# Optimization experiments

Measured on AMD Instinct MI355X. Metric: run time of the kernel, lower is better.

The kernel has to match this reference:

```python
import jax, jax.numpy as jnp
import numpy as np
from math import factorial

# ---- irreps metadata: 12x0e + 4x1o + 4x1e + 6x2e (dim 66) ----
GROUPS = [(12, 0), (4, 1), (4, 1), (6, 2)]  # (mul, l); parity: [e, o, e, e]

def _slices(groups):
    s, out = 0, []
    for m, l in groups:
        d = m * (2 * l + 1)
        out.append((s, s + d))
        s += d
    return out

SL = _slices(GROUPS)
DIM = SL[-1][1]                      # 66
SH_L = [0, 1, 2]
SH_SL = [(0, 1), (1, 4), (4, 9)]     # sh dim 9

# all parity/l-allowed paths (in_group, sh_idx, out_group) of the FC tensor product
PATHS = [(0, 0, 0), (0, 1, 1), (0, 2, 3),
         (1, 0, 1), (1, 1, 0), (1, 1, 2), (1, 1, 3), (1, 2, 1),
         (2, 0, 2), (2, 1, 1), (2, 2, 2), (2, 2, 3),
         (3, 0, 3), (3, 1, 1), (3, 2, 0), (3, 2, 2), (3, 2, 3)]
WEIGHT_NUMEL = sum(GROUPS[a][0] * GROUPS[c][0] for a, _, c in PATHS)  # 632
FAN = [0] * len(GROUPS)
for a, b, c in PATHS:
    FAN[c] += GROUPS[a][0]

# ---- real Clebsch-Gordan tensors ----

def _su2_cg(j1, j2, j3, m1, m2, m3):
    if m1 + m2 != m3:
        return 0.0
    f = factorial
    pre = ((2 * j3 + 1) * f(j3 + j1 - j2) * f(j3 - j1 + j2) * f(j1 + j2 - j3) / f(j1 + j2 + j3 + 1)) ** 0.5
    pre *= (f(j3 + m3) * f(j3 - m3) * f(j1 - m1) * f(j1 + m1) * f(j2 - m2) * f(j2 + m2)) ** 0.5
    s = 0.0
    for k in range(j1 + j2 - j3 + 1):
        args = (k, j1 + j2 - j3 - k, j1 - m1 - k, j2 + m2 - k, j3 - j2 + m1 + k, j3 - j1 - m2 + k)
        if min(args) < 0:
            continue
        d = 1.0
        for a in args:
            d *= f(a)
        s += (-1) ** k / d
    return pre * s

def _u_real(l):
    # complex -> real spherical-harmonic change of basis, rows m=-l..l
    U = np.zeros((2 * l + 1, 2 * l + 1), dtype=np.complex128)
    sq = 1.0 / np.sqrt(2.0)
    for m in range(-l, l + 1):
        i = m + l
        if m > 0:
            U[i, l + m] = ((-1) ** m) * sq
            U[i, l - m] = sq
        elif m == 0:
            U[i, l] = 1.0
        else:
            U[i, l + m] = 1j * sq
            U[i, l - m] = -1j * ((-1) ** m) * sq
    return U

def _real_cg(l1, l2, l3):
    Cc = np.zeros((2 * l1 + 1, 2 * l2 + 1, 2 * l3 + 1), dtype=np.complex128)
    for m1 in range(-l1, l1 + 1):
        for m2 in range(-l2, l2 + 1):
            m3 = m1 + m2
            if abs(m3) <= l3:
                Cc[l1 + m1, l2 + m2, l3 + m3] = _su2_cg(l1, l2, l3, m1, m2, m3)
    U1, U2, U3 = _u_real(l1), _u_real(l2), _u_real(l3)
    T = np.einsum('ai,bj,ck,ijk->abc', U1.conj(), U2.conj(), U3, Cc)
    T = T.real if np.abs(T.real).sum() >= np.abs(T.imag).sum() else T.imag
    T = T / np.linalg.norm(T)  # unit Frobenius norm
    return jnp.asarray(T.astype(np.float32))

CG = {k: _real_cg(*k) for k in {(GROUPS[a][1], SH_L[b], GROUPS[c][1]) for a, b, c in PATHS}}

# ---- equivariant building blocks ----

def irreps_linear(x, ws, b0):
    # block-diagonal linear over multiplicities; bias only on scalars (0e)
    outs = []
    for g, (m, l) in enumerate(GROUPS):
        xs = x[..., SL[g][0]:SL[g][1]].reshape(x.shape[:-1] + (m, 2 * l + 1))
        o = jnp.einsum('...ui,uv->...vi', xs, ws[g]) / np.sqrt(float(m))
        if l == 0:
            o = o + b0[:, None]
        outs.append(o.reshape(x.shape[:-1] + (m * (2 * l + 1),)))
    return jnp.concatenate(outs, axis=-1)

def sph_harm(r_hat):
    # component-normalized real SH up to l=2, l=1 in e3nn order (y, z, x)
    x, y, z = r_hat[..., 0], r_hat[..., 1], r_hat[..., 2]
    s3, s5, s15 = np.sqrt(3.0), np.sqrt(5.0), np.sqrt(15.0)
    Y0 = jnp.ones_like(x)[..., None]
    Y1 = s3 * jnp.stack([y, z, x], axis=-1)
    Y2 = jnp.stack([s15 * x * y, s15 * y * z, (s5 / 2) * (3 * z * z - 1),
                    s15 * x * z, (s15 / 2) * (x * x - y * y)], axis=-1)
    return jnp.concatenate([Y0, Y1, Y2], axis=-1)  # [..., 9]

def tensor_product(x, y, w):
    # x: [...,66] node feats, y: [...,9] SH, w: [...,632] per-edge weights
    outs = [None] * len(GROUPS)
    off = 0
    for a, b, c in PATHS:
        mul1, l1 = GROUPS[a]
        l2 = SH_L[b]
        mulo, lo = GROUPS[c]
        xs = x[..., SL[a][0]:SL[a][1]].reshape(x.shape[:-1] + (mul1, 2 * l1 + 1))
        ys = y[..., SH_SL[b][0]:SH_SL[b][1]]
        nw = mul1 * mulo
        ws = w[..., off:off + nw].reshape(w.shape[:-1] + (mul1, mulo))
        off += nw
        t = jnp.einsum('...ui,...j,ijk,...uv->...vk', xs, ys, CG[(l1, l2, lo)], ws)
        outs[c] = t if outs[c] is None else outs[c] + t
    res = []
    for c, (mulo, lo) in enumerate(GROUPS):
        alpha = np.sqrt(2.0 * lo + 1.0) / np.sqrt(float(FAN[c]))
        res.append((alpha * outs[c]).reshape(outs[c].shape[:-2] + (mulo * (2 * lo + 1),)))
    return jnp.concatenate(res, axis=-1)

def norm_act(x):
    # NormActivation: out = x * silu(||x||) / ||x|| per irrep channel
    outs = []
    for g, (m, l) in enumerate(GROUPS):
        xs = x[..., SL[g][0]:SL[g][1]].reshape(x.shape[:-1] + (m, 2 * l + 1))
        n = jnp.sqrt(jnp.sum(xs * xs, axis=-1, keepdims=True) + 1e-12)
        outs.append((xs * (jax.nn.silu(n) / n)).reshape(x.shape[:-1] + (m * (2 * l + 1),)))
    return jnp.concatenate(outs, axis=-1)

def _forward(h, e_src, e_dst, e_attr,
             lin_in_w0, lin_in_w1o, lin_in_w1e, lin_in_w2, lin_in_b0,
             res_w0, res_w1o, res_w1e, res_w2, res_b0, rad_w1, rad_w2):
    B, N, _ = h.shape
    E = e_attr.shape[1]
    h_in = irreps_linear(h, [lin_in_w0, lin_in_w1o, lin_in_w1e, lin_in_w2], lin_in_b0)
    h_src = jnp.take_along_axis(h_in, e_src[..., None], axis=1)          # [B,E,66]
    r_norm = jnp.linalg.norm(e_attr, axis=-1, keepdims=True) + 1e-8
    r_hat = e_attr / r_norm
    Y = sph_harm(r_hat)                                                  # [B,E,9]
    w = jax.nn.silu(r_norm @ rad_w1) @ rad_w2 / np.sqrt(float(rad_w2.shape[0]))  # [B,E,632]
    msg = tensor_product(h_src, Y, w)                                    # [B,E,66]
    flat_dst = (e_dst + jnp.arange(B, dtype=e_dst.dtype)[:, None] * N).reshape(-1)
    agg = jax.ops.segment_sum(msg.reshape(B * E, DIM), flat_dst, num_segments=B * N)
    agg = agg.reshape(B, N, DIM)
    h_out = agg + irreps_linear(h, [res_w0, res_w1o, res_w1e, res_w2], res_b0)
    return norm_act(h_out)

def setup_inputs() -> dict:
    key = jax.random.key(0)
    ks = jax.random.split(key, 16)
    B, N, E = 2, 20000, 50000
    return {
        'h': jax.random.normal(ks[0], (B, N, DIM), dtype=jnp.float32),
        'e_src': jax.random.randint(ks[1], (B, E), 0, N, dtype=jnp.int32),
        'e_dst': jax.random.randint(ks[2], (B, E), 0, N, dtype=jnp.int32),
        'e_attr': jax.random.normal(ks[3], (B, E, 3), dtype=jnp.float32),
        'lin_in_w0': jax.random.normal(ks[4], (12, 12), dtype=jnp.float32),
        'lin_in_w1o': jax.random.normal(ks[5], (4, 4), dtype=jnp.float32),
        'lin_in_w1e': jax.random.normal(ks[6], (4, 4), dtype=jnp.float32),
        'lin_in_w2': jax.random.normal(ks[7], (6, 6), dtype=jnp.float32),
        'lin_in_b0': jax.random.normal(ks[8], (12,), dtype=jnp.float32),
        'res_w0': jax.random.normal(ks[9], (12, 12), dtype=jnp.float32),
        'res_w1o': jax.random.normal(ks[10], (4, 4), dtype=jnp.float32),
        'res_w1e': jax.random.normal(ks[11], (4, 4), dtype=jnp.float32),
        'res_w2': jax.random.normal(ks[12], (6, 6), dtype=jnp.float32),
        'res_b0': jax.random.normal(ks[13], (12,), dtype=jnp.float32),
        'rad_w1': jax.random.normal(ks[14], (1, 32), dtype=jnp.float32),
        'rad_w2': jax.random.normal(ks[15], (32, WEIGHT_NUMEL), dtype=jnp.float32),
    }

def reference(h, e_src, e_dst, e_attr,
              lin_in_w0, lin_in_w1o, lin_in_w1e, lin_in_w2, lin_in_b0,
              res_w0, res_w1o, res_w1e, res_w2, res_b0, rad_w1, rad_w2):
    return _forward(h, e_src, e_dst, e_attr,
                    lin_in_w0, lin_in_w1o, lin_in_w1e, lin_in_w2, lin_in_b0,
                    res_w0, res_w1o, res_w1e, res_w2, res_b0, rad_w1, rad_w2)
```

## Files before the change

### kernel.cpp

```cpp
#include <hip/hip_runtime.h>
#include <math.h>

#define DIM 66
#define NPATH 17
#define WNUM 648
#define NHID 32

typedef _Float16 h2 __attribute__((ext_vector_type(2)));


__device__ double dfact(int n){ double f=1.0; for(int i=2;i<=n;i++) f*=(double)i; return f; }

__device__ double su2_cg(int j1,int j2,int j3,int m1,int m2,int m3){
  if(m1+m2!=m3) return 0.0;
  double pre = sqrt((double)(2*j3+1)*dfact(j3+j1-j2)*dfact(j3-j1+j2)*dfact(j1+j2-j3)/dfact(j1+j2+j3+1));
  pre *= sqrt(dfact(j3+m3)*dfact(j3-m3)*dfact(j1-m1)*dfact(j1+m1)*dfact(j2-m2)*dfact(j2+m2));
  double s=0.0;
  for(int k=0;k<=j1+j2-j3;k++){
    int a0=k, a1=j1+j2-j3-k, a2=j1-m1-k, a3=j2+m2-k, a4=j3-j2+m1+k, a5=j3-j1-m2+k;
    if(a0<0||a1<0||a2<0||a3<0||a4<0||a5<0) continue;
    double d = dfact(a0)*dfact(a1)*dfact(a2)*dfact(a3)*dfact(a4)*dfact(a5);
    s += ((k&1)? -1.0:1.0)/d;
  }
  return pre*s;
}

__device__ void u_real_entry(int l, int row, int col, double& re, double& im){
  re=0.0; im=0.0;
  const double sq = 0.7071067811865476;
  int m = row - l;
  if(m>0){
    if(col==l+m) re = ((m&1)? -sq : sq);
    else if(col==l-m) re = sq;
  } else if(m==0){
    if(col==l) re = 1.0;
  } else {
    int am = -m;
    if(col==l+m) im = sq;
    else if(col==l-m) im = ((am&1)? sq : -sq);
  }
}

__constant__ int c_l1[NPATH]   = {0,0,0,1,1,1,1,1,1,1,1,1,2,2,2,2,2};
__constant__ int c_l2[NPATH]   = {0,1,2,0,1,1,1,2,0,1,2,2,0,1,2,2,2};
__constant__ int c_l3[NPATH]   = {0,1,2,1,0,1,2,1,1,1,1,2,2,1,0,1,2};
__constant__ int c_cgoff[NPATH]= {0,1,10,35,44,53,80,125,170,179,206,251,326,351,396,421,496};

__global__ void cg_init_kernel(float* __restrict__ cg_out){
  int p = blockIdx.x;
  int l1=c_l1[p], l2=c_l2[p], l3=c_l3[p];
  int n1=2*l1+1, n2=2*l2+1, n3=2*l3+1;
  int ntot=n1*n2*n3;
  __shared__ double Cc[125];
  __shared__ double red[128];
  int t=threadIdx.x;
  if(t<ntot){
    int i=t/(n2*n3), j=(t/n3)%n2, k=t%n3;
    Cc[t] = su2_cg(l1,l2,l3,i-l1,j-l2,k-l3);
  }
  __syncthreads();
  double Tre=0.0, Tim=0.0;
  if(t<ntot){
    int a=t/(n2*n3), b=(t/n3)%n2, c=t%n3;
    for(int i=0;i<n1;i++)for(int j=0;j<n2;j++)for(int k=0;k<n3;k++){
      double cc=Cc[(i*n2+j)*n3+k];
      if(cc==0.0) continue;
      double u1r,u1i,u2r,u2i,u3r,u3i;
      u_real_entry(l1,a,i,u1r,u1i); u1i=-u1i;
      u_real_entry(l2,b,j,u2r,u2i); u2i=-u2i;
      u_real_entry(l3,c,k,u3r,u3i);
      double pr=u1r*u2r-u1i*u2i, pi=u1r*u2i+u1i*u2r;
      double qr=pr*u3r-pi*u3i,   qi=pr*u3i+pi*u3r;
      Tre+=qr*cc; Tim+=qi*cc;
    }
  }
  red[t]=fabs(Tre); __syncthreads();
  for(int s=64;s>0;s>>=1){ if(t<s) red[t]+=red[t+s]; __syncthreads(); }
  double sar=red[0]; __syncthreads();
  red[t]=fabs(Tim); __syncthreads();
  for(int s=64;s>0;s>>=1){ if(t<s) red[t]+=red[t+s]; __syncthreads(); }
  double sai=red[0]; __syncthreads();
  double chosen = (sar>=sai)? Tre : Tim;
  red[t]=chosen*chosen; __syncthreads();
  for(int s=64;s>0;s>>=1){ if(t<s) red[t]+=red[t+s]; __syncthreads(); }
  double nrm=sqrt(red[0]);
  if(t<ntot) cg_out[c_cgoff[p]+t] = (float)(chosen/nrm);
}


__global__ void wf2_pack_kernel(const float* __restrict__ w2, h2* __restrict__ wf2){
  int i=blockIdx.x*blockDim.x+threadIdx.x;
  if(i>=WNUM*16) return;
  int nr=i>>4, t2=i&15;
  const float sc = 0.17677669529663687f;
  h2 v;
  v.x = (_Float16)(w2[(2*t2  )*WNUM+nr]*sc);
  v.y = (_Float16)(w2[(2*t2+1)*WNUM+nr]*sc);
  wf2[i]=v;
}


__global__ void hid2_kernel(const float* __restrict__ e_attr, const float* __restrict__ rad_w1,
                            h2* __restrict__ hidg2, int BE){
  int el = blockIdx.x*blockDim.x+threadIdx.x;
  if(el>=BE) return;
  int t2 = blockIdx.y;
  const float* ea = e_attr + (long)el*3;
  float x=ea[0], y=ea[1], z=ea[2];
  float rn = sqrtf(x*x+y*y+z*z)+1e-8f;
  float a0 = rn*rad_w1[2*t2], a1 = rn*rad_w1[2*t2+1];
  h2 v;
  v.x = (_Float16)(a0/(1.f+expf(-a0)));
  v.y = (_Float16)(a1/(1.f+expf(-a1)));
  hidg2[(size_t)t2*BE + el] = v;
}


__global__ void linear_kernel(const float* __restrict__ h,
  const float* __restrict__ w0i, const float* __restrict__ w1oi, const float* __restrict__ w1ei,
  const float* __restrict__ w2i, const float* __restrict__ b0i,
  const float* __restrict__ w0r, const float* __restrict__ w1or_, const float* __restrict__ w1er,
  const float* __restrict__ w2r, const float* __restrict__ b0r,
  float* __restrict__ h_in, float* __restrict__ out, int total)
{
  int idx=blockIdx.x*blockDim.x+threadIdx.x;
  if(idx>=total) return;
  int d = idx % DIM;
  long bn = idx / DIM;
  const float* hr = h + bn*(long)DIM;
  float s1=0.f, s2=0.f, o1, o2;
  if(d<12){
    #pragma unroll
    for(int u=0;u<12;u++){ float xv=hr[u]; s1+=xv*w0i[u*12+d]; s2+=xv*w0r[u*12+d]; }
    const float r = 0.28867513459481287f;
    o1 = s1*r + b0i[d]; o2 = s2*r + b0r[d];
  } else if(d<24){
    int rel=d-12, v=rel/3, i=rel%3;
    #pragma unroll
    for(int u=0;u<4;u++){ float xv=hr[12+u*3+i]; s1+=xv*w1oi[u*4+v]; s2+=xv*w1or_[u*4+v]; }
    o1=s1*0.5f; o2=s2*0.5f;
  } else if(d<36){
    int rel=d-24, v=rel/3, i=rel%3;
    #pragma unroll
    for(int u=0;u<4;u++){ float xv=hr[24+u*3+i]; s1+=xv*w1ei[u*4+v]; s2+=xv*w1er[u*4+v]; }
    o1=s1*0.5f; o2=s2*0.5f;
  } else {
    int rel=d-36, v=rel/5, i=rel%5;
    #pragma unroll
    for(int u=0;u<6;u++){ float xv=hr[36+u*5+i]; s1+=xv*w2i[u*6+v]; s2+=xv*w2r[u*6+v]; }
    const float r=0.4082482904638631f;
    o1=s1*r; o2=s2*r;
  }
  h_in[idx]=o1; out[idx]=o2;
}


__global__ void count_kernel(const int* __restrict__ e_dst, int* __restrict__ cnt, int BE, int N, int E){
  int el=blockIdx.x*blockDim.x+threadIdx.x;
  if(el>=BE) return;
  int b=el/E;
  atomicAdd(&cnt[b*N+e_dst[el]], 1);
}

__global__ void scan_kernel(const int* __restrict__ cnt, int* __restrict__ off, int BN){
  __shared__ int part[1024];
  int t=threadIdx.x;
  int items=(BN+1023)>>10;
  int base=t*items;
  int s=0;
  for(int i=0;i<items;i++){ int idx=base+i; if(idx<BN) s+=cnt[idx]; }
  part[t]=s; __syncthreads();
  for(int d=1;d<1024;d<<=1){
    int v=(t>=d)?part[t-d]:0; __syncthreads();
    part[t]+=v; __syncthreads();
  }
  int run=(t==0)?0:part[t-1];
  for(int i=0;i<items;i++){ int idx=base+i; if(idx<BN){ off[idx]=run; run+=cnt[idx]; } }
}

__global__ void fill_kernel(const int* __restrict__ e_dst, const int* __restrict__ off,
                            int* __restrict__ cursor, int* __restrict__ elist, int BE, int N, int E){
  int el=blockIdx.x*blockDim.x+threadIdx.x;
  if(el>=BE) return;
  int b=el/E;
  int fd=b*N+e_dst[el];
  int pos=atomicAdd(&cursor[fd],1);
  elist[off[fd]+pos]=el;
}


template<int L1_,int L2_,int L3_,int MUL1,int MULO,int XOFF,int YOFF,int WOFF,int CGOFF>
__device__ __forceinline__ void do_path_f(const float* __restrict__ hs, const float* Y,
  const h2* __restrict__ wf2, const h2* __restrict__ hid2,
  const float* __restrict__ cgl, int v, float* acc)
{
  constexpr int N1=2*L1_+1, N2=2*L2_+1, N3=2*L3_+1;
  float M[N1*N3];
  #pragma unroll
  for(int i=0;i<N1;i++){
    #pragma unroll
    for(int k=0;k<N3;k++){
      float s=0.f;
      #pragma unroll
      for(int j=0;j<N2;j++) s += Y[YOFF+j]*cgl[CGOFF+(i*N2+j)*N3+k];
      M[i*N3+k]=s;
    }
  }
  #pragma unroll
  for(int u=0;u<MUL1;u++){
    const h2* wr = wf2 + (WOFF+u*MULO+v)*16;
    float w=0.f;
    #pragma unroll
    for(int t2=0;t2<16;t2++) w = __builtin_amdgcn_fdot2(wr[t2], hid2[t2], w, false);
    #pragma unroll
    for(int k=0;k<N3;k++){
      float z=0.f;
      #pragma unroll
      for(int i=0;i<N1;i++) z += hs[XOFF+u*N1+i]*M[i*N3+k];
      acc[k] += z*w;
    }
  }
}

template<bool USE_ATOMIC>
__global__ __launch_bounds__(256) void tp_out_kernel(
  const float* __restrict__ h_in, const int* __restrict__ e_src, const int* __restrict__ e_dst,
  const float* __restrict__ e_attr, const h2* __restrict__ hidg2, const h2* __restrict__ wf2,
  const float* __restrict__ cg, float* __restrict__ outdst, int BE, int N, int E)
{
  __shared__ float cgl[640];
  for(int i=threadIdx.x;i<621;i+=256) cgl[i]=cg[i];
  __syncthreads();
  long el = (long)blockIdx.y*256 + threadIdx.x;
  if(el>=BE) return;
  int vu = blockIdx.x;
  size_t BEs = (size_t)BE;
  int b = (int)(el / E);
  int src = e_src[el];
  const float* ea = e_attr + el*3;
  float x=ea[0], y=ea[1], z=ea[2];
  float rn = sqrtf(x*x+y*y+z*z) + 1e-8f;
  float xh=x/rn, yh=y/rn, zh=z/rn;
  float Y[9];
  const float s3=1.7320508075688772f, s5=2.23606797749979f, s15=3.872983346207417f;
  Y[0]=1.f; Y[1]=s3*yh; Y[2]=s3*zh; Y[3]=s3*xh;
  Y[4]=s15*xh*yh; Y[5]=s15*yh*zh; Y[6]=0.5f*s5*(3.f*zh*zh-1.f);
  Y[7]=s15*xh*zh; Y[8]=0.5f*s15*(xh*xh-yh*yh);
  h2 hid2[16];
  #pragma unroll
  for(int t2=0;t2<16;t2++) hid2[t2] = hidg2[(size_t)t2*BEs + el];
  const float* hs = h_in + ((long)b*N + src)*DIM;
  float* op = USE_ATOMIC ? (outdst + ((long)b*N + e_dst[el])*DIM) : nullptr;
  float acc[5];
  #pragma unroll
  for(int i=0;i<5;i++) acc[i]=0.f;

  if(vu<12){
    int v=vu;
    do_path_f<0,0,0,12,12,  0,0,   0,   0>(hs,Y,wf2,hid2,cgl,v,acc);
    do_path_f<1,1,0, 4,12, 12,1, 280,  44>(hs,Y,wf2,hid2,cgl,v,acc);
    do_path_f<2,2,0, 6,12, 36,4, 516, 396>(hs,Y,wf2,hid2,cgl,v,acc);
    float r = acc[0]*0.21320071635561044f;
    if(USE_ATOMIC) unsafeAtomicAdd(&op[v], r);
    else outdst[(size_t)v*BEs + el] = r;
  } else if(vu<16){
    int v=vu-12;
    do_path_f<0,1,1,12, 4,  0,1, 144,   1>(hs,Y,wf2,hid2,cgl,v,acc);
    do_path_f<1,0,1, 4, 4, 12,0, 264,  35>(hs,Y,wf2,hid2,cgl,v,acc);
    do_path_f<1,2,1, 4, 4, 12,4, 368, 125>(hs,Y,wf2,hid2,cgl,v,acc);
    do_path_f<1,1,1, 4, 4, 24,1, 400, 179>(hs,Y,wf2,hid2,cgl,v,acc);
    do_path_f<2,1,1, 6, 4, 36,1, 492, 351>(hs,Y,wf2,hid2,cgl,v,acc);
    #pragma unroll
    for(int k=0;k<3;k++){
      float r = acc[k]*0.31622776601683794f;
      int d = 12+v*3+k;
      if(USE_ATOMIC) unsafeAtomicAdd(&op[d], r);
      else outdst[(size_t)d*BEs + el] = r;
    }
  } else if(vu<20){
    int v=vu-16;
    do_path_f<1,1,1, 4, 4, 12,1, 328,  53>(hs,Y,wf2,hid2,cgl,v,acc);
    do_path_f<1,0,1, 4, 4, 24,0, 384, 170>(hs,Y,wf2,hid2,cgl,v,acc);
    do_path_f<1,2,1, 4, 4, 24,4, 416, 206>(hs,Y,wf2,hid2,cgl,v,acc);
    do_path_f<2,2,1, 6, 4, 36,4, 588, 421>(hs,Y,wf2,hid2,cgl,v,acc);
    #pragma unroll
    for(int k=0;k<3;k++){
      float r = acc[k]*0.4082482904638631f;
      int d = 24+v*3+k;
      if(USE_ATOMIC) unsafeAtomicAdd(&op[d], r);
      else outdst[(size_t)d*BEs + el] = r;
    }
  } else {
    int v=vu-20;
    do_path_f<0,2,2,12, 6,  0,4, 192,  10>(hs,Y,wf2,hid2,cgl,v,acc);
    do_path_f<1,1,2, 4, 6, 12,1, 344,  80>(hs,Y,wf2,hid2,cgl,v,acc);
    do_path_f<1,2,2, 4, 6, 24,4, 432, 251>(hs,Y,wf2,hid2,cgl,v,acc);
    do_path_f<2,0,2, 6, 6, 36,0, 456, 326>(hs,Y,wf2,hid2,cgl,v,acc);
    do_path_f<2,2,2, 6, 6, 36,4, 612, 496>(hs,Y,wf2,hid2,cgl,v,acc);
    #pragma unroll
    for(int k=0;k<5;k++){
      float r = acc[k]*0.3952847075210474f;
      int d = 36+v*5+k;
      if(USE_ATOMIC) unsafeAtomicAdd(&op[d], r);
      else outdst[(size_t)d*BEs + el] = r;
    }
  }
}


__global__ __launch_bounds__(256) void msg_tr_kernel(
  const float* __restrict__ msg, float* __restrict__ msgT, int BE)
{
  __shared__ float tile[DIM*65];
  long e0 = (long)blockIdx.x*64;
  for(int i=threadIdx.x;i<DIM*64;i+=256){
    int d=i>>6, e=i&63;
    long el=e0+e;
    tile[d*65+e] = (el<BE)? msg[(size_t)d*BE+el] : 0.f;
  }
  __syncthreads();
  for(int i=threadIdx.x;i<64*DIM;i+=256){
    int e=i/DIM, d=i-e*DIM;
    long el=e0+e;
    if(el<BE) msgT[(size_t)el*DIM+d] = tile[d*65+e];
  }
}


__global__ __launch_bounds__(256) void gather2_kernel(
  const float* __restrict__ msgT, const int* __restrict__ cnt, const int* __restrict__ off,
  const int* __restrict__ elist, float* __restrict__ out, int BN)
{
  int wave = threadIdx.x>>6, lane = threadIdx.x&63;
  long node = (long)blockIdx.x*4 + wave;
  if(node>=BN) return;
  int c = cnt[node], o = off[node];
  float s0=0.f, s1=0.f;
  for(int i=0;i<c;i++){
    int el = elist[o+i];
    const float* mr = msgT + (size_t)el*DIM;
    s0 += mr[lane];
    if(lane<2) s1 += mr[64+lane];
  }
  float* op = out + node*(long)DIM;
  op[lane] += s0;
  if(lane<2) op[64+lane] += s1;
}


__global__ void norm_act_kernel(float* __restrict__ out, int total){
  int idx=blockIdx.x*blockDim.x+threadIdx.x;
  if(idx>=total) return;
  int c = idx % 26; long bn = idx / 26;
  int off, len;
  if(c<12){ off=c; len=1; }
  else if(c<16){ off=12+(c-12)*3; len=3; }
  else if(c<20){ off=24+(c-16)*3; len=3; }
  else { off=36+(c-20)*5; len=5; }
  float* p = out + bn*(long)DIM + off;
  float sum=0.f;
  for(int i=0;i<len;i++){ float v=p[i]; sum+=v*v; }
  float n = sqrtf(sum+1e-12f);
  float sc = 1.f/(1.f+expf(-n));
  for(int i=0;i<len;i++) p[i]*=sc;
}


extern "C" void kernel_launch(void* const* d_in, const int* in_sizes, int n_in,
                              void* d_out, int out_size, void* d_ws, size_t ws_size,
                              hipStream_t stream)
{
  const float* h       = (const float*)d_in[0];
  const int*   e_src   = (const int*)  d_in[1];
  const int*   e_dst   = (const int*)  d_in[2];
  const float* e_attr  = (const float*)d_in[3];
  const float* lw0     = (const float*)d_in[4];
  const float* lw1o    = (const float*)d_in[5];
  const float* lw1e    = (const float*)d_in[6];
  const float* lw2     = (const float*)d_in[7];
  const float* lb0     = (const float*)d_in[8];
  const float* rw0     = (const float*)d_in[9];
  const float* rw1o    = (const float*)d_in[10];
  const float* rw1e    = (const float*)d_in[11];
  const float* rw2     = (const float*)d_in[12];
  const float* rb0     = (const float*)d_in[13];
  const float* rad_w1  = (const float*)d_in[14];
  const float* rad_w2  = (const float*)d_in[15];

  const int B  = 2;
  const int BE = in_sizes[1];
  const int E  = BE / B;
  const int BN = in_sizes[0] / DIM;
  const int N  = BN / B;

  float* ws   = (float*)d_ws;
  float* h_in = ws;
  float* cg   = ws + (size_t)BN*DIM;
  h2*    wf2  = (h2*)(cg + 640);
  h2*    hidg2= wf2 + (size_t)WNUM*16;
  float* msg  = (float*)(hidg2 + (size_t)16*BE);
  float* msgT = msg + (size_t)DIM*BE;
  int*   cnt  = (int*)(msgT + (size_t)BE*DIM);
  int*   cur  = cnt + BN;
  int*   offp = cur + BN;
  int*   elist= offp + BN;

  size_t need_f = (size_t)BN*DIM + 640 + (size_t)WNUM*16 + (size_t)16*BE
                + 2*(size_t)DIM*BE + 3*(size_t)BN + (size_t)BE;
  bool csr_ok = (ws_size/4) >= need_f + 1024;

  cg_init_kernel<<<NPATH, 128, 0, stream>>>(cg);
  int wfn = WNUM*16;
  wf2_pack_kernel<<<(wfn+255)/256, 256, 0, stream>>>(rad_w2, wf2);
  dim3 hgrid((BE+255)/256, 16);
  hid2_kernel<<<hgrid, 256, 0, stream>>>(e_attr, rad_w1, hidg2, BE);
  int totL = BN*DIM;
  linear_kernel<<<(totL+255)/256, 256, 0, stream>>>(h, lw0, lw1o, lw1e, lw2, lb0,
                                                    rw0, rw1o, rw1e, rw2, rb0,
                                                    h_in, (float*)d_out, totL);
  if(csr_ok){
    hipMemsetAsync(cnt, 0, 2*(size_t)BN*sizeof(int), stream);
    count_kernel<<<(BE+255)/256, 256, 0, stream>>>(e_dst, cnt, BE, N, E);
    scan_kernel<<<1, 1024, 0, stream>>>(cnt, offp, BN);
    fill_kernel<<<(BE+255)/256, 256, 0, stream>>>(e_dst, offp, cur, elist, BE, N, E);
    dim3 bgrid(26, (BE+255)/256);
    tp_out_kernel<false><<<bgrid, 256, 0, stream>>>(h_in, e_src, e_dst, e_attr,
                                                    hidg2, wf2, cg, msg, BE, N, E);
    msg_tr_kernel<<<(BE+63)/64, 256, 0, stream>>>(msg, msgT, BE);
    gather2_kernel<<<(BN+3)/4, 256, 0, stream>>>(msgT, cnt, offp, elist, (float*)d_out, BN);
  } else {
    dim3 bgrid(26, (BE+255)/256);
    tp_out_kernel<true><<<bgrid, 256, 0, stream>>>(h_in, e_src, e_dst, e_attr,
                                                   hidg2, wf2, cg, (float*)d_out, BE, N, E);
  }
  int totN = BN*26;
  norm_act_kernel<<<(totN+255)/256, 256, 0, stream>>>((float*)d_out, totN);
}
```

Before: 308.0 us.

## Store edge messages in fp16 and fuse gated norm activation into gather

Per-edge messages are written as fp16 instead of fp32, which halves the bytes moved through tp_out, the transpose kernel and the gather. The gather kernel now also applies the per-irrep norm-sigmoid gate via a shared-memory tile, so the separate norm_act launch and its extra pass over the output are skipped on the CSR path. This reduces precision of the summed messages, and the shared-memory reads in the gate have no barrier, relying on each wave writing only its own row.

Measured after the change: 297.3 us. 3.5% less time.

```diff
diff --git a/kernel.cpp b/kernel.cpp
--- a/kernel.cpp
+++ b/kernel.cpp
@@ -226,7 +226,8 @@
 __global__ __launch_bounds__(256) void tp_out_kernel(
   const float* __restrict__ h_in, const int* __restrict__ e_src, const int* __restrict__ e_dst,
   const float* __restrict__ e_attr, const h2* __restrict__ hidg2, const h2* __restrict__ wf2,
-  const float* __restrict__ cg, float* __restrict__ outdst, int BE, int N, int E)
+  const float* __restrict__ cg, float* __restrict__ outat, _Float16* __restrict__ msgh,
+  int BE, int N, int E)
 {
   __shared__ float cgl[640];
   for(int i=threadIdx.x;i<621;i+=256) cgl[i]=cg[i];
@@ -250,7 +251,7 @@
   #pragma unroll
   for(int t2=0;t2<16;t2++) hid2[t2] = hidg2[(size_t)t2*BEs + el];
   const float* hs = h_in + ((long)b*N + src)*DIM;
-  float* op = USE_ATOMIC ? (outdst + ((long)b*N + e_dst[el])*DIM) : nullptr;
+  float* op = USE_ATOMIC ? (outat + ((long)b*N + e_dst[el])*DIM) : nullptr;
   float acc[5];
   #pragma unroll
   for(int i=0;i<5;i++) acc[i]=0.f;
@@ -262,7 +263,7 @@
     do_path_f<2,2,0, 6,12, 36,4, 516, 396>(hs,Y,wf2,hid2,cgl,v,acc);
     float r = acc[0]*0.21320071635561044f;
     if(USE_ATOMIC) unsafeAtomicAdd(&op[v], r);
-    else outdst[(size_t)v*BEs + el] = r;
+    else msgh[(size_t)v*BEs + el] = (_Float16)r;
   } else if(vu<16){
     int v=vu-12;
     do_path_f<0,1,1,12, 4,  0,1, 144,   1>(hs,Y,wf2,hid2,cgl,v,acc);
@@ -275,7 +276,7 @@
       float r = acc[k]*0.31622776601683794f;
       int d = 12+v*3+k;
       if(USE_ATOMIC) unsafeAtomicAdd(&op[d], r);
-      else outdst[(size_t)d*BEs + el] = r;
+      else msgh[(size_t)d*BEs + el] = (_Float16)r;
     }
   } else if(vu<20){
     int v=vu-16;
@@ -288,7 +289,7 @@
       float r = acc[k]*0.4082482904638631f;
       int d = 24+v*3+k;
       if(USE_ATOMIC) unsafeAtomicAdd(&op[d], r);
-      else outdst[(size_t)d*BEs + el] = r;
+      else msgh[(size_t)d*BEs + el] = (_Float16)r;
     }
   } else {
     int v=vu-20;
@@ -302,35 +303,36 @@
       float r = acc[k]*0.3952847075210474f;
       int d = 36+v*5+k;
       if(USE_ATOMIC) unsafeAtomicAdd(&op[d], r);
-      else outdst[(size_t)d*BEs + el] = r;
+      else msgh[(size_t)d*BEs + el] = (_Float16)r;
     }
   }
 }
 
 
 __global__ __launch_bounds__(256) void msg_tr_kernel(
-  const float* __restrict__ msg, float* __restrict__ msgT, int BE)
-{
-  __shared__ float tile[DIM*65];
+  const _Float16* __restrict__ msgh, _Float16* __restrict__ msgT, int BE)
+{
+  __shared__ _Float16 tile[DIM*66];
   long e0 = (long)blockIdx.x*64;
   for(int i=threadIdx.x;i<DIM*64;i+=256){
     int d=i>>6, e=i&63;
     long el=e0+e;
-    tile[d*65+e] = (el<BE)? msg[(size_t)d*BE+el] : 0.f;
+    tile[d*66+e] = (el<BE)? msgh[(size_t)d*BE+el] : (_Float16)0.f;
   }
   __syncthreads();
   for(int i=threadIdx.x;i<64*DIM;i+=256){
     int e=i/DIM, d=i-e*DIM;
     long el=e0+e;
-    if(el<BE) msgT[(size_t)el*DIM+d] = tile[d*65+e];
+    if(el<BE) msgT[(size_t)el*DIM+d] = tile[d*66+e];
   }
 }
 
 
 __global__ __launch_bounds__(256) void gather2_kernel(
-  const float* __restrict__ msgT, const int* __restrict__ cnt, const int* __restrict__ off,
+  const _Float16* __restrict__ msgT, const int* __restrict__ cnt, const int* __restrict__ off,
   const int* __restrict__ elist, float* __restrict__ out, int BN)
 {
+  __shared__ float tot[4][DIM];
   int wave = threadIdx.x>>6, lane = threadIdx.x&63;
   long node = (long)blockIdx.x*4 + wave;
   if(node>=BN) return;
@@ -338,13 +340,35 @@
   float s0=0.f, s1=0.f;
   for(int i=0;i<c;i++){
     int el = elist[o+i];
-    const float* mr = msgT + (size_t)el*DIM;
-    s0 += mr[lane];
-    if(lane<2) s1 += mr[64+lane];
+    const _Float16* mr = msgT + (size_t)el*DIM;
+    s0 += (float)mr[lane];
+    if(lane<2) s1 += (float)mr[64+lane];
   }
   float* op = out + node*(long)DIM;
-  op[lane] += s0;
-  if(lane<2) op[64+lane] += s1;
+  float t0 = op[lane] + s0;
+  tot[wave][lane] = t0;
+  float t1 = 0.f;
+  if(lane<2){ t1 = op[64+lane] + s1; tot[wave][64+lane] = t1; }
+  {
+    int d = lane, offc, len;
+    if(d<12){ offc=d; len=1; }
+    else if(d<24){ offc=12+((d-12)/3)*3; len=3; }
+    else if(d<36){ offc=24+((d-24)/3)*3; len=3; }
+    else { offc=36+((d-36)/5)*5; len=5; }
+    float ss=0.f;
+    for(int i=0;i<len;i++){ float v=tot[wave][offc+i]; ss+=v*v; }
+    float n = sqrtf(ss+1e-12f);
+    float sc = 1.f/(1.f+expf(-n));
+    op[d] = t0*sc;
+  }
+  if(lane<2){
+    int d = 64+lane;
+    float ss=0.f;
+    for(int i=0;i<5;i++){ float v=tot[wave][61+i]; ss+=v*v; }
+    float n = sqrtf(ss+1e-12f);
+    float sc = 1.f/(1.f+expf(-n));
+    op[d] = t1*sc;
+  }
 }
 
 
@@ -398,15 +422,15 @@
   float* cg   = ws + (size_t)BN*DIM;
   h2*    wf2  = (h2*)(cg + 640);
   h2*    hidg2= wf2 + (size_t)WNUM*16;
-  float* msg  = (float*)(hidg2 + (size_t)16*BE);
-  float* msgT = msg + (size_t)DIM*BE;
+  _Float16* msgh = (_Float16*)(hidg2 + (size_t)16*BE);
+  _Float16* msgT = msgh + (size_t)DIM*BE;
   int*   cnt  = (int*)(msgT + (size_t)BE*DIM);
   int*   cur  = cnt + BN;
   int*   offp = cur + BN;
   int*   elist= offp + BN;
 
   size_t need_f = (size_t)BN*DIM + 640 + (size_t)WNUM*16 + (size_t)16*BE
-                + 2*(size_t)DIM*BE + 3*(size_t)BN + (size_t)BE;
+                + (size_t)DIM*BE + 3*(size_t)BN + (size_t)BE;
   bool csr_ok = (ws_size/4) >= need_f + 1024;
 
   cg_init_kernel<<<NPATH, 128, 0, stream>>>(cg);
@@ -425,14 +449,14 @@
     fill_kernel<<<(BE+255)/256, 256, 0, stream>>>(e_dst, offp, cur, elist, BE, N, E);
     dim3 bgrid(26, (BE+255)/256);
     tp_out_kernel<false><<<bgrid, 256, 0, stream>>>(h_in, e_src, e_dst, e_attr,
-                                                    hidg2, wf2, cg, msg, BE, N, E);
-    msg_tr_kernel<<<(BE+63)/64, 256, 0, stream>>>(msg, msgT, BE);
+                                                    hidg2, wf2, cg, nullptr, msgh, BE, N, E);
+    msg_tr_kernel<<<(BE+63)/64, 256, 0, stream>>>(msgh, msgT, BE);
     gather2_kernel<<<(BN+3)/4, 256, 0, stream>>>(msgT, cnt, offp, elist, (float*)d_out, BN);
   } else {
     dim3 bgrid(26, (BE+255)/256);
     tp_out_kernel<true><<<bgrid, 256, 0, stream>>>(h_in, e_src, e_dst, e_attr,
-                                                   hidg2, wf2, cg, (float*)d_out, BE, N, E);
-  }
-  int totN = BN*26;
-  norm_act_kernel<<<(totN+255)/256, 256, 0, stream>>>((float*)d_out, totN);
-}
+                                                   hidg2, wf2, cg, (float*)d_out, msgh, BE, N, E);
+    int totN = BN*26;
+    norm_act_kernel<<<(totN+255)/256, 256, 0, stream>>>((float*)d_out, totN);
+  }
+}
```
